# Performance work log

Hardware: AMD Instinct MI355X
Metric: run time of the kernel (lower is better)

Reference implementation:

```python
import jax, jax.numpy as jnp
import numpy as np

H = 4  # n_heads in nn.MultiheadAttention
LN_EPS = 1e-5


def _mha_seq1(x_q, x_kv, in_w, in_b, out_w, out_b):
    """torch nn.MultiheadAttention with batch_first and seq_len=1 on q and kv.
    x_q, x_kv: [B, F]. in_w: [3F, F] (packed q/k/v), out_w: [F, F].
    With a single kv position, softmax over the kv axis is identically 1,
    so the output equals out_proj(v); we still compute scores/softmax so the
    math (and zero grads to Wq/Wk) matches torch exactly.
    """
    B, F = x_q.shape
    dh = F // H
    wq, wk, wv = jnp.split(in_w, 3, axis=0)
    bq, bk, bv = jnp.split(in_b, 3, axis=0)
    q = (x_q @ wq.T + bq).reshape(B, H, dh)
    k = (x_kv @ wk.T + bk).reshape(B, H, dh)
    v = (x_kv @ wv.T + bv).reshape(B, H, dh)
    s = jnp.einsum('bhd,bhd->bh', q, k) / jnp.sqrt(jnp.asarray(dh, x_q.dtype))
    w = jax.nn.softmax(s[..., None], axis=-1)  # [B, H, 1] == 1
    o = (w * v).reshape(B, F)
    return o @ out_w.T + out_b


def _layer_norm(x, g, b):
    mu = jnp.mean(x, axis=-1, keepdims=True)
    var = jnp.mean(jnp.square(x - mu), axis=-1, keepdims=True)
    return (x - mu) * jax.lax.rsqrt(var + LN_EPS) * g + b


def setup_inputs() -> dict:
    key = jax.random.key(0)
    B, GD, TD, F = 16384, 1024, 1024, 2048
    ks = jax.random.split(key, 20)
    s = 0.02  # weight init scale
    return {
        'graph_feat': jax.random.normal(ks[0], (B, GD), jnp.float32),
        'temporal_feat': jax.random.normal(ks[1], (B, TD), jnp.float32),
        'gp_w': jax.random.normal(ks[2], (F, GD), jnp.float32) * s,
        'gp_b': jax.random.normal(ks[3], (F,), jnp.float32) * s,
        'tp_w': jax.random.normal(ks[4], (F, TD), jnp.float32) * s,
        'tp_b': jax.random.normal(ks[5], (F,), jnp.float32) * s,
        'in1_w': jax.random.normal(ks[6], (3 * F, F), jnp.float32) * s,
        'in1_b': jax.random.normal(ks[7], (3 * F,), jnp.float32) * s,
        'out1_w': jax.random.normal(ks[8], (F, F), jnp.float32) * s,
        'out1_b': jax.random.normal(ks[9], (F,), jnp.float32) * s,
        'in2_w': jax.random.normal(ks[10], (3 * F, F), jnp.float32) * s,
        'in2_b': jax.random.normal(ks[11], (3 * F,), jnp.float32) * s,
        'out2_w': jax.random.normal(ks[12], (F, F), jnp.float32) * s,
        'out2_b': jax.random.normal(ks[13], (F,), jnp.float32) * s,
        'gate_w': jax.random.normal(ks[14], (F, 2 * F), jnp.float32) * s,
        'gate_b': jax.random.normal(ks[15], (F,), jnp.float32) * s,
        'ln_g': jnp.ones((F,), jnp.float32),
        'ln_b': jnp.zeros((F,), jnp.float32),
        'lin_w': jax.random.normal(ks[16], (F, F), jnp.float32) * s,
        'lin_b': jax.random.normal(ks[17], (F,), jnp.float32) * s,
    }


def reference(graph_feat, temporal_feat, gp_w, gp_b, tp_w, tp_b,
              in1_w, in1_b, out1_w, out1_b, in2_w, in2_b, out2_w, out2_b,
              gate_w, gate_b, ln_g, ln_b, lin_w, lin_b):
    g = graph_feat @ gp_w.T + gp_b          # [B, F]
    t = temporal_feat @ tp_w.T + tp_b       # [B, F]
    attn1 = _mha_seq1(g, t, in1_w, in1_b, out1_w, out1_b)  # cross1(g, t, t)
    attn2 = _mha_seq1(t, g, in2_w, in2_b, out2_w, out2_b)  # cross2(t, g, g)
    cross = attn1 + attn2
    gate = jax.nn.sigmoid(jnp.concatenate([g, cross], axis=-1) @ gate_w.T + gate_b)
    fused = gate * g + (1.0 - gate) * cross
    fused = _layer_norm(fused + g, ln_g, ln_b)
    return fused @ lin_w.T + lin_b
```

## Files before the change

### kernel.cpp

```cpp
#include <hip/hip_runtime.h>
#include <stdint.h>

typedef __attribute__((ext_vector_type(8))) short short8;
typedef __attribute__((ext_vector_type(4))) float f32x4;

__device__ __forceinline__ unsigned short f2bf(float f) {
  union { float f; uint32_t u; } v; v.f = f;
  uint32_t u = v.u;
  u += 0x7FFF + ((u >> 16) & 1);
  return (unsigned short)(u >> 16);
}
__device__ __forceinline__ float bf2f(unsigned short h) {
  union { uint32_t u; float f; } v; v.u = ((uint32_t)h) << 16;
  return v.f;
}

__global__ void conv_kernel(const float* __restrict__ in,
                            unsigned short* __restrict__ out, int n) {
  long i = ((long)blockIdx.x * blockDim.x + threadIdx.x) * 8;
  if (i >= n) return;
  float4 a = *(const float4*)(in + i);
  float4 b = *(const float4*)(in + i + 4);
  short8 s;
  s[0] = (short)f2bf(a.x); s[1] = (short)f2bf(a.y);
  s[2] = (short)f2bf(a.z); s[3] = (short)f2bf(a.w);
  s[4] = (short)f2bf(b.x); s[5] = (short)f2bf(b.y);
  s[6] = (short)f2bf(b.z); s[7] = (short)f2bf(b.w);
  *(short8*)(out + i) = s;
}

__global__ void convcat_kernel(const float* __restrict__ in,
                               unsigned short* __restrict__ out,
                               int colbase, int n) {
  long i = ((long)blockIdx.x * blockDim.x + threadIdx.x) * 8;
  if (i >= n) return;
  float4 a = *(const float4*)(in + i);
  float4 b = *(const float4*)(in + i + 4);
  short8 s;
  s[0] = (short)f2bf(a.x); s[1] = (short)f2bf(a.y);
  s[2] = (short)f2bf(a.z); s[3] = (short)f2bf(a.w);
  s[4] = (short)f2bf(b.x); s[5] = (short)f2bf(b.y);
  s[6] = (short)f2bf(b.z); s[7] = (short)f2bf(b.w);
  long row = i >> 10, col = i & 1023;
  *(short8*)(out + row * 2048 + colbase + col) = s;
}

__global__ void convs_kernel(const float* __restrict__ in,
                             const float* __restrict__ scale,
                             unsigned short* __restrict__ out, int n) {
  long i = ((long)blockIdx.x * blockDim.x + threadIdx.x) * 8;
  if (i >= n) return;
  short8 s;
#pragma unroll
  for (int j = 0; j < 8; ++j)
    s[j] = (short)f2bf(in[i + j] * scale[(i + j) & 2047]);
  *(short8*)(out + i) = s;
}

__global__ void tconv_kernel(const float* __restrict__ in, int R, int C,
                             unsigned short* __restrict__ out) {
  __shared__ float tile[32][33];
  int c0 = blockIdx.x * 32, r0 = blockIdx.y * 32;
  int tx = threadIdx.x, ty = threadIdx.y;
#pragma unroll
  for (int i = 0; i < 32; i += 8)
    tile[ty + i][tx] = in[(long)(r0 + ty + i) * C + c0 + tx];
  __syncthreads();
#pragma unroll
  for (int i = 0; i < 32; i += 8)
    out[(long)(c0 + ty + i) * R + r0 + tx] = f2bf(tile[tx][ty + i]);
}

enum { CE_PLAIN = 0, CE_WT = 1, CE_ACC = 2 };

template <int CE>
__global__ __launch_bounds__(256)
void compose_kernel(const unsigned short* __restrict__ A, int lda,
                    const unsigned short* __restrict__ W, int ldw,
                    unsigned short* C, int ldc,
                    unsigned short* Ct, long ctoff,
                    int K, int nmt,
                    int pairBase, long aoff, long woff, long coff) {
  constexpr int BK = 32;
  __shared__ unsigned short sA[128 * BK];
  __shared__ unsigned short sB[128 * BK];
  const int tid  = threadIdx.x;
  const int lane = tid & 63;
  const int wave = tid >> 6;
  const int wr = (wave >> 1) * 64;
  const int wc = (wave & 1) * 64;

  int bid = blockIdx.x;
  if (bid >= pairBase) {
    bid -= pairBase;
    A += aoff; W += woff; C += coff; Ct += ctoff;
  }
  const long tileM = (long)(bid % nmt) * 128;
  const long tileN = (long)(bid / nmt) * 128;

  const unsigned short* gA = A + (tileM + (tid >> 2)) * (long)lda + (tid & 3) * 8;
  const unsigned short* gB = W + (tileN + (tid >> 2)) * (long)ldw + (tid & 3) * 8;
  unsigned short* lA = sA + wave * 512;
  unsigned short* lB = sB + wave * 512;

  f32x4 acc[4][4] = {};
  const int fr = lane & 15;
  const int kb = (lane >> 4) * 8;

  for (int k0 = 0; k0 < K; k0 += BK) {
    __builtin_amdgcn_global_load_lds(
        (const __attribute__((address_space(1))) void*)(gA + k0),
        (__attribute__((address_space(3))) void*)(lA), 16, 0, 0);
    __builtin_amdgcn_global_load_lds(
        (const __attribute__((address_space(1))) void*)(gA + k0 + 64 * (long)lda),
        (__attribute__((address_space(3))) void*)(lA + 2048), 16, 0, 0);
    __builtin_amdgcn_global_load_lds(
        (const __attribute__((address_space(1))) void*)(gB + k0),
        (__attribute__((address_space(3))) void*)(lB), 16, 0, 0);
    __builtin_amdgcn_global_load_lds(
        (const __attribute__((address_space(1))) void*)(gB + k0 + 64 * (long)ldw),
        (__attribute__((address_space(3))) void*)(lB + 2048), 16, 0, 0);
    __syncthreads();

    short8 aF[4], bF[4];
#pragma unroll
    for (int m = 0; m < 4; ++m)
      aF[m] = *(const short8*)&sA[(wr + m * 16 + fr) * BK + kb];
#pragma unroll
    for (int n = 0; n < 4; ++n)
      bF[n] = *(const short8*)&sB[(wc + n * 16 + fr) * BK + kb];
#pragma unroll
    for (int m = 0; m < 4; ++m)
#pragma unroll
      for (int n = 0; n < 4; ++n)
        acc[m][n] = __builtin_amdgcn_mfma_f32_16x16x32_bf16(aF[m], bF[n], acc[m][n], 0, 0, 0);
    __syncthreads();
  }

  const int cr = (lane >> 4) * 4;
  const int cc = lane & 15;
#pragma unroll
  for (int m = 0; m < 4; ++m) {
    long r0 = tileM + wr + m * 16 + cr;
#pragma unroll
    for (int n = 0; n < 4; ++n) {
      long c = tileN + wc + n * 16 + cc;
#pragma unroll
      for (int r = 0; r < 4; ++r) {
        long idx = (r0 + r) * (long)ldc + c;
        float v = acc[m][n][r];
        if constexpr (CE == CE_ACC) v += bf2f(C[idx]);
        unsigned short bv = f2bf(v);
        C[idx] = bv;
        if constexpr (CE == CE_WT) Ct[c * 2048 + (r0 + r)] = bv;
      }
    }
  }
}

enum { EPI_BIAS = 0, EPI_LNF32 = 4 };

#define VMW(N) asm volatile("s_waitcnt vmcnt(" #N ")" ::: "memory")
#define SBAR() __builtin_amdgcn_s_barrier()

template <int EPI>
__global__ __launch_bounds__(512, 4)
void gemm128_kernel(const unsigned short* __restrict__ A, int lda,
                    const unsigned short* __restrict__ W, int ldw,
                    int K, int ldc, int nmt,
                    const float* __restrict__ bias,
                    const float* __restrict__ bias2,
                    const float2* __restrict__ stats,
                    void* Cv) {
  __shared__ unsigned short smem[32768];

  const int tid = threadIdx.x, lane = tid & 63, w = tid >> 6;
  const int wm = w >> 2, wn = w & 3;

  const int q = nmt >> 3;
  const int xcd = blockIdx.x & 7, seq = blockIdx.x >> 3;
  const int mt = xcd * q + (seq % q);
  const int nt = seq / q;
  const long tileM = (long)mt * 128, tileN = (long)nt * 128;

  const int sRow = w * 16 + (lane >> 3);
  const int sCol = (((lane & 7) ^ ((lane >> 3) & 7)) * 8);
  const unsigned short* pSA = A + (tileM + sRow) * (long)lda + sCol;
  const unsigned short* pSB = W + (tileN + sRow) * (long)ldw + sCol;
  const long lda8 = 8 * (long)lda, ldw8 = 8 * (long)ldw;

  const int fr = lane & 15, kc = lane >> 4, l7 = lane & 7;
  const unsigned aOff0 = (wm * 64 + fr) * 128 + ((kc) ^ l7) * 16;
  const unsigned aOff1 = (wm * 64 + fr) * 128 + ((4 + kc) ^ l7) * 16;
  const unsigned bOff0 = 16384 + (wn * 32 + fr) * 128 + ((kc) ^ l7) * 16;
  const unsigned bOff1 = 16384 + (wn * 32 + fr) * 128 + ((4 + kc) ^ l7) * 16;

  f32x4 acc[4][2] = {};

#define STGK(D)                                                               \
  { char* la_ = (char*)smem + (D) * 32768 + w * 2048;                         \
    char* lb_ = la_ + 16384;                                                  \
    __builtin_amdgcn_global_load_lds(                                         \
        (const __attribute__((address_space(1))) void*)pSA,                   \
        (__attribute__((address_space(3))) void*)la_, 16, 0, 0);              \
    __builtin_amdgcn_global_load_lds(                                         \
        (const __attribute__((address_space(1))) void*)(pSA + lda8),          \
        (__attribute__((address_space(3))) void*)(la_ + 1024), 16, 0, 0);     \
    __builtin_amdgcn_global_load_lds(                                         \
        (const __attribute__((address_space(1))) void*)pSB,                   \
        (__attribute__((address_space(3))) void*)lb_, 16, 0, 0);              \
    __builtin_amdgcn_global_load_lds(                                         \
        (const __attribute__((address_space(1))) void*)(pSB + ldw8),          \
        (__attribute__((address_space(3))) void*)(lb_ + 1024), 16, 0, 0);     \
    pSA += 64; pSB += 64; }

#define ITER(D, LAST)                                                         \
  {                                                                           \
    if (!(LAST)) STGK((D) ^ 1);                                               \
    short8 aF[4][2], bF[2][2];                                                \
    const char* ba = (const char*)smem + (D) * 32768;                         \
    _Pragma("unroll") for (int m = 0; m < 4; ++m) {                           \
      aF[m][0] = *(const short8*)(ba + aOff0 + m * 2048);                     \
      aF[m][1] = *(const short8*)(ba + aOff1 + m * 2048);                     \
    }                                                                         \
    _Pragma("unroll") for (int n = 0; n < 2; ++n) {                           \
      bF[n][0] = *(const short8*)(ba + bOff0 + n * 2048);                     \
      bF[n][1] = *(const short8*)(ba + bOff1 + n * 2048);                     \
    }                                                                         \
    __builtin_amdgcn_s_setprio(1);                                            \
    _Pragma("unroll") for (int m = 0; m < 4; ++m)                             \
    _Pragma("unroll") for (int n = 0; n < 2; ++n) {                           \
      acc[m][n] = __builtin_amdgcn_mfma_f32_16x16x32_bf16(                    \
          aF[m][0], bF[n][0], acc[m][n], 0, 0, 0);                            \
      acc[m][n] = __builtin_amdgcn_mfma_f32_16x16x32_bf16(                    \
          aF[m][1], bF[n][1], acc[m][n], 0, 0, 0);                            \
    }                                                                         \
    __builtin_amdgcn_s_setprio(0);                                            \
    asm volatile("s_waitcnt lgkmcnt(0)" ::: "memory");                        \
    if (!(LAST)) VMW(0);                                                      \
    SBAR();                                                                   \
  }

  STGK(0);
  VMW(0);
  SBAR();

  const int NT = K / 64;
  for (int kt = 0; kt < NT - 2; kt += 2) {
    ITER(0, 0);
    ITER(1, 0);
  }
  ITER(0, 0);
  ITER(1, 1);
#undef ITER
#undef STGK

  const int cr = (lane >> 4) * 4;
  const int cc = lane & 15;
#pragma unroll
  for (int m = 0; m < 4; ++m) {
    long rr = tileM + wm * 64 + m * 16 + cr;
#pragma unroll
    for (int n = 0; n < 2; ++n) {
      long c = tileN + wn * 32 + n * 16 + cc;
      float b1 = bias ? bias[c] : 0.0f;
      float b2 = bias2 ? bias2[c] : 0.0f;
#pragma unroll
      for (int r = 0; r < 4; ++r) {
        long row = rr + r;
        long idx = row * (long)ldc + c;
        float v = acc[m][n][r];
        if constexpr (EPI == EPI_BIAS) {
          ((unsigned short*)Cv)[idx] = f2bf(v + b1 + b2);
        }
        if constexpr (EPI == EPI_LNF32) {
          float2 st = stats[row];
          ((float*)Cv)[idx] = v * st.y - st.y * st.x * b1 + b2;
        }
      }
    }
  }
}

__global__ __launch_bounds__(256) void fusestats_kernel(
    const unsigned short* __restrict__ CL, const unsigned short* __restrict__ G,
    unsigned short* __restrict__ PL, float2* __restrict__ stats) {
  const int row = blockIdx.x;
  const int t = threadIdx.x, lane = t & 63, wave = t >> 6;
  short8 xc = *(const short8*)&CL[(long)row * 4096 + t * 8];
  short8 xl = *(const short8*)&CL[(long)row * 4096 + 2048 + t * 8];
  short8 xg = *(const short8*)&G[(long)row * 2048 + t * 8];
  short8 o8;
  float s = 0.f, s2 = 0.f;
#pragma unroll
  for (int j = 0; j < 8; ++j) {
    float cv = bf2f((unsigned short)xc[j]);
    float lv = bf2f((unsigned short)xl[j]);
    float gv = bf2f((unsigned short)xg[j]);
    float gt = 1.0f / (1.0f + expf(-lv));
    unsigned short pb = f2bf(gt * gv + (1.0f - gt) * cv + gv);
    o8[j] = (short)pb;
    float x = bf2f(pb);
    s += x; s2 += x * x;
  }
  *(short8*)(PL + (long)row * 2048 + t * 8) = o8;
#pragma unroll
  for (int off = 1; off < 64; off <<= 1) {
    s  += __shfl_xor(s, off);
    s2 += __shfl_xor(s2, off);
  }
  __shared__ float red[8];
  if (lane == 0) { red[wave] = s; red[4 + wave] = s2; }
  __syncthreads();
  if (t == 0) {
    float ts  = red[0] + red[1] + red[2] + red[3];
    float ts2 = red[4] + red[5] + red[6] + red[7];
    float mean = ts * (1.0f / 2048.0f);
    float var  = ts2 * (1.0f / 2048.0f) - mean * mean;
    stats[row] = make_float2(mean, rsqrtf(var + 1e-5f));
  }
}

__device__ __forceinline__ float blkRed(float s, float* red, int lane, int wave) {
#pragma unroll
  for (int off = 1; off < 64; off <<= 1) s += __shfl_xor(s, off);
  if (lane == 0) red[wave] = s;
  __syncthreads();
  return red[0] + red[1] + red[2] + red[3];
}

__global__ __launch_bounds__(256) void biascompP_kernel(
    const unsigned short* __restrict__ wO1b, const unsigned short* __restrict__ wO2b,
    const unsigned short* __restrict__ Wc1, const unsigned short* __restrict__ Wc2,
    const float* __restrict__ bv1, const float* __restrict__ bv2,
    const float* __restrict__ tpb, const float* __restrict__ gpb,
    const float* __restrict__ o1b, const float* __restrict__ o2b,
    float* __restrict__ bcV) {
  __shared__ float red[4];
  int c = blockIdx.x, t = threadIdx.x, lane = t & 63, wave = t >> 6;
  int k = t * 8;
  float s = 0.f;
  short8 a1 = *(const short8*)(wO1b + (long)c * 2048 + k);
  short8 a2 = *(const short8*)(wO2b + (long)c * 2048 + k);
  short8 a3 = *(const short8*)(Wc1 + (long)c * 2048 + k);
  short8 a4 = *(const short8*)(Wc2 + (long)c * 2048 + k);
#pragma unroll
  for (int j = 0; j < 8; ++j)
    s += bf2f((unsigned short)a1[j]) * bv1[k + j]
       + bf2f((unsigned short)a2[j]) * bv2[k + j]
       + bf2f((unsigned short)a3[j]) * tpb[k + j]
       + bf2f((unsigned short)a4[j]) * gpb[k + j];
  float tot = blkRed(s, red, lane, wave);
  if (t == 0) bcV[c] = tot + o1b[c] + o2b[c];
}

__global__ __launch_bounds__(256) void bgateP_kernel(
    const float* __restrict__ gate_w, const float* __restrict__ gate_b,
    const float* __restrict__ gpb, const float* __restrict__ bcV,
    float* __restrict__ bgateV) {
  __shared__ float red[4];
  int n = blockIdx.x, t = threadIdx.x, lane = t & 63, wave = t >> 6;
  const float* row = gate_w + (long)n * 4096;
  float s = 0.f;
  int k = t * 8;
#pragma unroll
  for (int j = 0; j < 8; ++j)
    s += row[k + j] * gpb[k + j] + row[2048 + k + j] * bcV[k + j];
  float tot = blkRed(s, red, lane, wave);
  if (t == 0) bgateV[n] = tot + gate_b[n];
}

__global__ __launch_bounds__(256) void uvP_kernel(
    const unsigned short* __restrict__ wlinp, const float* __restrict__ lin_w,
    const float* __restrict__ ln_beta, const float* __restrict__ lin_b,
    float* __restrict__ uV, float* __restrict__ vV) {
  __shared__ float redu[4], redv[4];
  int n = blockIdx.x, t = threadIdx.x, lane = t & 63, wave = t >> 6;
  int k = t * 8;
  short8 a1 = *(const short8*)(wlinp + (long)n * 2048 + k);
  float u = 0.f, v = 0.f;
#pragma unroll
  for (int j = 0; j < 8; ++j) {
    u += bf2f((unsigned short)a1[j]);
    v += ln_beta[k + j] * lin_w[(long)n * 2048 + k + j];
  }
#pragma unroll
  for (int off = 1; off < 64; off <<= 1) {
    u += __shfl_xor(u, off);
    v += __shfl_xor(v, off);
  }
  if (lane == 0) { redu[wave] = u; redv[wave] = v; }
  __syncthreads();
  if (t == 0) {
    uV[n] = redu[0] + redu[1] + redu[2] + redu[3];
    vV[n] = redv[0] + redv[1] + redv[2] + redv[3] + lin_b[n];
  }
}

extern "C" void kernel_launch(void* const* d_in, const int* in_sizes, int n_in,
                              void* d_out, int out_size, void* d_ws, size_t ws_size,
                              hipStream_t stream) {
  const float* graph    = (const float*)d_in[0];
  const float* temporal = (const float*)d_in[1];
  const float* gp_w  = (const float*)d_in[2];
  const float* gp_b  = (const float*)d_in[3];
  const float* tp_w  = (const float*)d_in[4];
  const float* tp_b  = (const float*)d_in[5];
  const float* in1_w = (const float*)d_in[6];
  const float* in1_b = (const float*)d_in[7];
  const float* out1_w = (const float*)d_in[8];
  const float* out1_b = (const float*)d_in[9];
  const float* in2_w = (const float*)d_in[10];
  const float* in2_b = (const float*)d_in[11];
  const float* out2_w = (const float*)d_in[12];
  const float* out2_b = (const float*)d_in[13];
  const float* gate_w = (const float*)d_in[14];
  const float* gate_b = (const float*)d_in[15];
  const float* ln_g  = (const float*)d_in[16];
  const float* ln_b  = (const float*)d_in[17];
  const float* lin_w = (const float*)d_in[18];
  const float* lin_b = (const float*)d_in[19];

  const int Bm = 16384, F = 2048, GD = 1024;
  const long BF = (long)Bm * F, FF = (long)F * F, FG = (long)F * GD;

  unsigned short* TG   = (unsigned short*)d_ws;
  unsigned short* PL   = TG;
  unsigned short* Gbuf = TG + BF;
  unsigned short* wLIN = Gbuf + BF;
  unsigned short* wGP  = wLIN + FF;
  unsigned short* Wcg  = wGP + FG;
  unsigned short* Wcross = Wcg;
  unsigned short* Wgate  = Wcg + FF;
  float* bc2V   = (float*)(Wcg + 2 * FF);
  float* uV     = bc2V + 2 * F;
  float* vV     = uV + F;
  float2* stats = (float2*)(vV + F);

  unsigned short* DO      = (unsigned short*)d_out;
  unsigned short* wv1T    = DO;
  unsigned short* wv2T    = wv1T + FF;
  unsigned short* tpT     = wv2T + FF;
  unsigned short* gpT     = tpT + FG;
  unsigned short* Wc1     = gpT + FG;
  unsigned short* Wc2     = Wc1 + FF;
  unsigned short* wO1b    = Wc2 + FF;
  unsigned short* wO2b    = wO1b + FF;
  unsigned short* wGATEb  = wO2b + FF;
  unsigned short* WcrossT = wGATEb + 2 * FF;
  unsigned short* CL      = DO;

  auto conv = [&](const float* src, unsigned short* dst, long n) {
    conv_kernel<<<dim3((unsigned)(n / 8 / 256)), 256, 0, stream>>>(src, dst, (int)n);
  };
  convcat_kernel<<<dim3((unsigned)(Bm * GD / 8 / 256)), 256, 0, stream>>>(
      temporal, TG, 0, Bm * GD);
  convcat_kernel<<<dim3((unsigned)(Bm * GD / 8 / 256)), 256, 0, stream>>>(
      graph, TG, GD, Bm * GD);
  conv(gp_w, wGP, FG);
  conv(out1_w, wO1b, FF);
  conv(out2_w, wO2b, FF);
  conv(gate_w, wGATEb, 2 * FF);
  convs_kernel<<<dim3((unsigned)(FF / 8 / 256)), 256, 0, stream>>>(lin_w, ln_g, wLIN, (int)FF);
  tconv_kernel<<<dim3(F / 32, F / 32), dim3(32, 8), 0, stream>>>(in1_w + 2 * FF, F, F, wv1T);
  tconv_kernel<<<dim3(F / 32, F / 32), dim3(32, 8), 0, stream>>>(in2_w + 2 * FF, F, F, wv2T);
  tconv_kernel<<<dim3(GD / 32, F / 32), dim3(32, 8), 0, stream>>>(tp_w, F, GD, tpT);
  tconv_kernel<<<dim3(GD / 32, F / 32), dim3(32, 8), 0, stream>>>(gp_w, F, GD, gpT);

  compose_kernel<CE_PLAIN><<<dim3(512), dim3(256), 0, stream>>>(
      wO1b, F, wv1T, F, Wc1, F, nullptr, 0, F, 16,
      256, wO2b - wO1b, wv2T - wv1T, Wc2 - Wc1);
  compose_kernel<CE_WT><<<dim3(256), dim3(256), 0, stream>>>(
      Wc1, F, tpT, F, Wcross, F, WcrossT, (long)1024 * 2048, F, 16,
      128, Wc2 - Wc1, gpT - tpT, 1024);
  biascompP_kernel<<<dim3(F), dim3(256), 0, stream>>>(
      wO1b, wO2b, Wc1, Wc2, in1_b + 2 * F, in2_b + 2 * F, tp_b, gp_b,
      out1_b, out2_b, bc2V);
  compose_kernel<CE_PLAIN><<<dim3(256), dim3(256), 0, stream>>>(
      wGATEb + F, 2 * F, WcrossT, F, Wgate, F, nullptr, 0, F, 16,
      1 << 30, 0, 0, 0);
  compose_kernel<CE_ACC><<<dim3(128), dim3(256), 0, stream>>>(
      wGATEb, 2 * F, gpT, F, Wgate + GD, F, nullptr, 0, F, 16,
      1 << 30, 0, 0, 0);
  bgateP_kernel<<<dim3(F), dim3(256), 0, stream>>>(gate_w, gate_b, gp_b, bc2V,
                                                   bc2V + F);
  uvP_kernel<<<dim3(F), dim3(256), 0, stream>>>(wLIN, lin_w, ln_b, lin_b, uV, vV);

  dim3 blk(512);
  const int NMT = Bm / 128;
  gemm128_kernel<EPI_BIAS><<<dim3(NMT * (F / 128)), blk, 0, stream>>>(
      TG + GD, F, wGP, GD, GD, F, NMT,
      gp_b, nullptr, nullptr, Gbuf);
  gemm128_kernel<EPI_BIAS><<<dim3(NMT * (2 * F / 128)), blk, 0, stream>>>(
      TG, F, Wcg, F, F, 2 * F, NMT,
      bc2V, nullptr, nullptr, CL);
  fusestats_kernel<<<dim3(Bm), dim3(256), 0, stream>>>(CL, Gbuf, PL, stats);
  gemm128_kernel<EPI_LNF32><<<dim3(NMT * (F / 128)), blk, 0, stream>>>(
      PL, F, wLIN, F, F, F, NMT,
      uV, vV, stats, (void*)d_out);
}
```

Before: 911.6 us.

## Switch main GEMMs to 256x256 tiles with 4 waves and 128x128 per-wave subtiles

```diff
diff --git a/kernel.cpp b/kernel.cpp
--- a/kernel.cpp
+++ b/kernel.cpp
@@ -164,105 +164,102 @@
 #define SBAR() __builtin_amdgcn_s_barrier()
 
 template <int EPI>
-__global__ __launch_bounds__(512, 4)
-void gemm128_kernel(const unsigned short* __restrict__ A, int lda,
-                    const unsigned short* __restrict__ W, int ldw,
-                    int K, int ldc, int nmt,
-                    const float* __restrict__ bias,
-                    const float* __restrict__ bias2,
-                    const float2* __restrict__ stats,
-                    void* Cv) {
-  __shared__ unsigned short smem[32768];
-
+__global__ __launch_bounds__(256, 1)
+void gemm4w_kernel(const unsigned short* __restrict__ A, int lda,
+                   const unsigned short* __restrict__ W, int ldw,
+                   int K, int ldc,
+                   const float* __restrict__ bias,
+                   const float* __restrict__ bias2,
+                   const float2* __restrict__ stats,
+                   void* Cv) {
+  __shared__ unsigned short smem[65536];
+  char* smc = (char*)smem;
   const int tid = threadIdx.x, lane = tid & 63, w = tid >> 6;
-  const int wm = w >> 2, wn = w & 3;
-
-  const int q = nmt >> 3;
+  const int wm = w >> 1, wn = w & 1;
+
   const int xcd = blockIdx.x & 7, seq = blockIdx.x >> 3;
-  const int mt = xcd * q + (seq % q);
-  const int nt = seq / q;
-  const long tileM = (long)mt * 128, tileN = (long)nt * 128;
-
-  const int sRow = w * 16 + (lane >> 3);
+  const int mt = xcd * 8 + (seq & 7);
+  const int nt = seq >> 3;
+  const long tileM = (long)mt * 256, tileN = (long)nt * 256;
+
+  const int sRow = w * 64 + (lane >> 3);
   const int sCol = (((lane & 7) ^ ((lane >> 3) & 7)) * 8);
   const unsigned short* pSA = A + (tileM + sRow) * (long)lda + sCol;
   const unsigned short* pSB = W + (tileN + sRow) * (long)ldw + sCol;
   const long lda8 = 8 * (long)lda, ldw8 = 8 * (long)ldw;
 
   const int fr = lane & 15, kc = lane >> 4, l7 = lane & 7;
-  const unsigned aOff0 = (wm * 64 + fr) * 128 + ((kc) ^ l7) * 16;
-  const unsigned aOff1 = (wm * 64 + fr) * 128 + ((4 + kc) ^ l7) * 16;
-  const unsigned bOff0 = 16384 + (wn * 32 + fr) * 128 + ((kc) ^ l7) * 16;
-  const unsigned bOff1 = 16384 + (wn * 32 + fr) * 128 + ((4 + kc) ^ l7) * 16;
-
-  f32x4 acc[4][2] = {};
-
-#define STGK(D)                                                               \
-  { char* la_ = (char*)smem + (D) * 32768 + w * 2048;                         \
-    char* lb_ = la_ + 16384;                                                  \
-    __builtin_amdgcn_global_load_lds(                                         \
-        (const __attribute__((address_space(1))) void*)pSA,                   \
-        (__attribute__((address_space(3))) void*)la_, 16, 0, 0);              \
-    __builtin_amdgcn_global_load_lds(                                         \
-        (const __attribute__((address_space(1))) void*)(pSA + lda8),          \
-        (__attribute__((address_space(3))) void*)(la_ + 1024), 16, 0, 0);     \
-    __builtin_amdgcn_global_load_lds(                                         \
-        (const __attribute__((address_space(1))) void*)pSB,                   \
-        (__attribute__((address_space(3))) void*)lb_, 16, 0, 0);              \
-    __builtin_amdgcn_global_load_lds(                                         \
-        (const __attribute__((address_space(1))) void*)(pSB + ldw8),          \
-        (__attribute__((address_space(3))) void*)(lb_ + 1024), 16, 0, 0);     \
+  const unsigned aOff0 = (wm * 128 + fr) * 128 + ((kc) ^ l7) * 16;
+  const unsigned aOff1 = (wm * 128 + fr) * 128 + ((4 + kc) ^ l7) * 16;
+  const unsigned bOff0 = 32768 + (wn * 128 + fr) * 128 + ((kc) ^ l7) * 16;
+  const unsigned bOff1 = 32768 + (wn * 128 + fr) * 128 + ((4 + kc) ^ l7) * 16;
+
+  f32x4 acc[8][8] = {};
+
+#define STG4(D)                                                               \
+  { const unsigned short* a_ = pSA; const unsigned short* b_ = pSB;           \
+    char* la_ = smc + (D) * 65536 + w * 8192;                                 \
+    char* lb_ = la_ + 32768;                                                  \
+    _Pragma("unroll") for (int j = 0; j < 8; ++j) {                           \
+      __builtin_amdgcn_global_load_lds(                                       \
+          (const __attribute__((address_space(1))) void*)a_,                  \
+          (__attribute__((address_space(3))) void*)(la_ + j * 1024), 16,0,0); \
+      a_ += lda8;                                                             \
+    }                                                                         \
+    _Pragma("unroll") for (int j = 0; j < 8; ++j) {                           \
+      __builtin_amdgcn_global_load_lds(                                       \
+          (const __attribute__((address_space(1))) void*)b_,                  \
+          (__attribute__((address_space(3))) void*)(lb_ + j * 1024), 16,0,0); \
+      b_ += ldw8;                                                             \
+    }                                                                         \
     pSA += 64; pSB += 64; }
 
-#define ITER(D, LAST)                                                         \
+#define PHASE4(D, LAST)                                                       \
   {                                                                           \
-    if (!(LAST)) STGK((D) ^ 1);                                               \
-    short8 aF[4][2], bF[2][2];                                                \
-    const char* ba = (const char*)smem + (D) * 32768;                         \
-    _Pragma("unroll") for (int m = 0; m < 4; ++m) {                           \
+    VMW(0);          \
+    SBAR();                                                                   \
+    short8 aF[8][2], bF[8][2];                                                \
+    const char* ba = smc + (D) * 65536;                                       \
+    _Pragma("unroll") for (int m = 0; m < 8; ++m) {                           \
       aF[m][0] = *(const short8*)(ba + aOff0 + m * 2048);                     \
       aF[m][1] = *(const short8*)(ba + aOff1 + m * 2048);                     \
     }                                                                         \
-    _Pragma("unroll") for (int n = 0; n < 2; ++n) {                           \
+    _Pragma("unroll") for (int n = 0; n < 8; ++n) {                           \
       bF[n][0] = *(const short8*)(ba + bOff0 + n * 2048);                     \
       bF[n][1] = *(const short8*)(ba + bOff1 + n * 2048);                     \
     }                                                                         \
+    if (!(LAST)) STG4((D) ^ 1);                                               \
     __builtin_amdgcn_s_setprio(1);                                            \
-    _Pragma("unroll") for (int m = 0; m < 4; ++m)                             \
-    _Pragma("unroll") for (int n = 0; n < 2; ++n) {                           \
+    _Pragma("unroll") for (int m = 0; m < 8; ++m)                             \
+    _Pragma("unroll") for (int n = 0; n < 8; ++n) {                           \
       acc[m][n] = __builtin_amdgcn_mfma_f32_16x16x32_bf16(                    \
           aF[m][0], bF[n][0], acc[m][n], 0, 0, 0);                            \
       acc[m][n] = __builtin_amdgcn_mfma_f32_16x16x32_bf16(                    \
           aF[m][1], bF[n][1], acc[m][n], 0, 0, 0);                            \
     }                                                                         \
     __builtin_amdgcn_s_setprio(0);                                            \
-    asm volatile("s_waitcnt lgkmcnt(0)" ::: "memory");                        \
-    if (!(LAST)) VMW(0);                                                      \
     SBAR();                                                                   \
   }
 
-  STGK(0);
-  VMW(0);
-  SBAR();
-
+  STG4(0);
   const int NT = K / 64;
-  for (int kt = 0; kt < NT - 2; kt += 2) {
-    ITER(0, 0);
-    ITER(1, 0);
-  }
-  ITER(0, 0);
-  ITER(1, 1);
-#undef ITER
-#undef STGK
+  for (int t = 0; t < NT - 2; t += 2) {
+    PHASE4(0, 0);
+    PHASE4(1, 0);
+  }
+  PHASE4(0, 0);
+  PHASE4(1, 1);
+#undef PHASE4
+#undef STG4
 
   const int cr = (lane >> 4) * 4;
   const int cc = lane & 15;
 #pragma unroll
-  for (int m = 0; m < 4; ++m) {
-    long rr = tileM + wm * 64 + m * 16 + cr;
-#pragma unroll
-    for (int n = 0; n < 2; ++n) {
-      long c = tileN + wn * 32 + n * 16 + cc;
+  for (int m = 0; m < 8; ++m) {
+    long rr = tileM + wm * 128 + m * 16 + cr;
+#pragma unroll
+    for (int n = 0; n < 8; ++n) {
+      long c = tileN + wn * 128 + n * 16 + cc;
       float b1 = bias ? bias[c] : 0.0f;
       float b2 = bias2 ? bias2[c] : 0.0f;
 #pragma unroll
@@ -486,16 +483,15 @@
                                                    bc2V + F);
   uvP_kernel<<<dim3(F), dim3(256), 0, stream>>>(wLIN, lin_w, ln_b, lin_b, uV, vV);
 
-  dim3 blk(512);
-  const int NMT = Bm / 128;
-  gemm128_kernel<EPI_BIAS><<<dim3(NMT * (F / 128)), blk, 0, stream>>>(
-      TG + GD, F, wGP, GD, GD, F, NMT,
+  dim3 blk(256);
+  gemm4w_kernel<EPI_BIAS><<<dim3(512), blk, 0, stream>>>(
+      TG + GD, F, wGP, GD, GD, F,
       gp_b, nullptr, nullptr, Gbuf);
-  gemm128_kernel<EPI_BIAS><<<dim3(NMT * (2 * F / 128)), blk, 0, stream>>>(
-      TG, F, Wcg, F, F, 2 * F, NMT,
+  gemm4w_kernel<EPI_BIAS><<<dim3(1024), blk, 0, stream>>>(
+      TG, F, Wcg, F, F, 2 * F,
       bc2V, nullptr, nullptr, CL);
   fusestats_kernel<<<dim3(Bm), dim3(256), 0, stream>>>(CL, Gbuf, PL, stats);
-  gemm128_kernel<EPI_LNF32><<<dim3(NMT * (F / 128)), blk, 0, stream>>>(
-      PL, F, wLIN, F, F, F, NMT,
+  gemm4w_kernel<EPI_LNF32><<<dim3(512), blk, 0, stream>>>(
+      PL, F, wLIN, F, F, F,
       uV, vV, stats, (void*)d_out);
 }
```

After: 864.4 us. -5.2%, faster.
